# Performance work log

Measured on AMD Instinct MI355X. Metric: run time of the kernel, lower is better.

Reference implementation:

```python
import jax, jax.numpy as jnp
import numpy as np

B, S, DIM = 2, 2048, 1536
H = 12            # n_heads (SIGMA)
HD = DIM // H     # head_dim = 128
SIGMA = 12        # anchors per query: 6 local + 4 strided + 2 global
STRIDE_STEP = 5   # SOPFR


def setup_inputs() -> dict:
    key = jax.random.key(0)
    k0, k1, k2 = jax.random.split(key, 3)
    s = 0.02
    return {
        "x": jax.random.normal(k0, (B, S, DIM), dtype=jnp.float32),
        "Wqkv": jax.random.normal(k1, (DIM, 3 * DIM), dtype=jnp.float32) * s,
        "bqkv": jnp.zeros((3 * DIM,), dtype=jnp.float32),
        "Wout": jax.random.normal(k2, (DIM, DIM), dtype=jnp.float32) * s,
        "bout": jnp.zeros((DIM,), dtype=jnp.float32),
        # Egyptian-fraction init: [W_LOCAL, W_STRIDE, W_GLOBAL] = [1/2, 1/3, 1/6]
        "group_scale": jnp.array([0.5, 1.0 / 3.0, 1.0 / 6.0], dtype=jnp.float32),
    }


def _anchor_indices(seq_len):
    # (S, 12) int32: 6 local offsets, 4 strided offsets, then global {0, S-1}
    pos = jnp.arange(seq_len, dtype=jnp.int32)
    offs = jnp.array([-3, -2, -1, 1, 2, 3,
                      -2 * STRIDE_STEP, -STRIDE_STEP, STRIDE_STEP, 2 * STRIDE_STEP],
                     dtype=jnp.int32)
    a = jnp.clip(pos[:, None] + offs[None, :], 0, seq_len - 1)
    glob = jnp.stack([jnp.zeros_like(pos), jnp.full_like(pos, seq_len - 1)], axis=1)
    return jnp.concatenate([a, glob], axis=1)


def reference(x, Wqkv, bqkv, Wout, bout, group_scale):
    b, s, d_model = x.shape
    # QKV projection -> (3, B, H, S, HD)
    qkv = (x @ Wqkv + bqkv).reshape(b, s, 3, H, HD).transpose(2, 0, 3, 1, 4)
    q, k, v = qkv[0], qkv[1], qkv[2]
    scale = HD ** -0.5

    anchor = _anchor_indices(s)                 # (S, SIGMA)
    k_anchors = jnp.take(k, anchor, axis=2)     # (B, H, S, SIGMA, HD)
    v_anchors = jnp.take(v, anchor, axis=2)     # (B, H, S, SIGMA, HD)

    attn = jnp.einsum('bhsd,bhsad->bhsa', q, k_anchors) * scale

    gw = jax.nn.softmax(group_scale)            # (3,)
    weight_per_anchor = jnp.concatenate([
        jnp.broadcast_to(gw[0], (6,)),   # local
        jnp.broadcast_to(gw[1], (4,)),   # strided
        jnp.broadcast_to(gw[2], (2,)),   # global
    ])                                          # (SIGMA,)
    attn = attn + jnp.log(weight_per_anchor)    # broadcast over (B,H,S,·)

    attn = jax.nn.softmax(attn, axis=-1)
    attn = jnp.nan_to_num(attn, nan=0.0)

    out = jnp.einsum('bhsa,bhsad->bhsd', attn, v_anchors)
    out = out.transpose(0, 2, 1, 3).reshape(b, s, d_model)
    return out @ Wout + bout
```

## Files before the change

### kernel.cpp

```cpp
#include <hip/hip_runtime.h>
#include <hip/hip_bf16.h>
#include <cstdint>
#include <math.h>

#define B_    2
#define S_    2048
#define DIM_  1536
#define H_    12
#define HD_   128
#define TRI_  4608
#define M_    4096

typedef __attribute__((ext_vector_type(8)))  __bf16 bf16x8;
typedef __attribute__((ext_vector_type(4)))  __bf16 bf16x4;
typedef __attribute__((ext_vector_type(4)))  float  floatx4;
typedef __attribute__((ext_vector_type(16))) float  floatx16;

typedef __attribute__((address_space(3))) uint8_t       lds_u8;
typedef const __attribute__((address_space(1))) uint8_t glob_u8;

__global__ __launch_bounds__(256) void prep(const float* __restrict__ W1,
                                            __bf16* __restrict__ O1,
                                            const float* __restrict__ W2,
                                            __bf16* __restrict__ O2,
                                            const float* __restrict__ x,
                                            __bf16* __restrict__ x_bf) {
    const int T1 = (TRI_ / 64) * (DIM_ / 64);
    const int T2 = (DIM_ / 64) * (DIM_ / 64);
    int blk = blockIdx.x;
    const int t = threadIdx.x;

    if (blk >= T1 + T2) {
        blk -= T1 + T2;
        int i = blk * 256 + t;
        float4 v = ((const float4*)x)[i];
        bf16x4 o;
        o.x = (__bf16)v.x; o.y = (__bf16)v.y; o.z = (__bf16)v.z; o.w = (__bf16)v.w;
        *(bf16x4*)(x_bf + (size_t)i * 4) = o;
        return;
    }

    const float* in; __bf16* out; int R, C, c0, r0;
    if (blk < T1) {
        in = W1; out = O1; R = DIM_; C = TRI_;
        c0 = (blk % (TRI_ / 64)) * 64; r0 = (blk / (TRI_ / 64)) * 64;
    } else {
        blk -= T1;
        in = W2; out = O2; R = DIM_; C = DIM_;
        c0 = (blk % (DIM_ / 64)) * 64; r0 = (blk / (DIM_ / 64)) * 64;
    }
    __shared__ float tile[64][65];
    const int c4 = t & 15, r = t >> 4;
    #pragma unroll
    for (int i = 0; i < 64; i += 16) {
        float4 v = *(const float4*)&in[(size_t)(r0 + r + i) * C + c0 + c4 * 4];
        tile[r + i][c4 * 4 + 0] = v.x;
        tile[r + i][c4 * 4 + 1] = v.y;
        tile[r + i][c4 * 4 + 2] = v.z;
        tile[r + i][c4 * 4 + 3] = v.w;
    }
    __syncthreads();
    const int cc = t >> 2, ch = t & 3;
    #pragma unroll
    for (int cho = 0; cho < 8; cho += 4) {
        int chh = ch + cho;
        bf16x8 o;
        #pragma unroll
        for (int k = 0; k < 8; ++k) o[k] = (__bf16)tile[chh * 8 + k][cc];
        *(bf16x8*)&out[(size_t)(c0 + cc) * R + r0 + chh * 8] = o;
    }
}

__global__ __launch_bounds__(256, 3) void gemm_qkv(const __bf16* __restrict__ A,
                                                   const __bf16* __restrict__ Bt,
                                                   const float*  __restrict__ bias,
                                                   __bf16* __restrict__ Cout,
                                                   int Mdim, int Ndim, int Kdim) {
    __shared__ __align__(16) __bf16 sA[128 * 64];
    __shared__ __align__(16) __bf16 sB[192 * 64];

    const int ntiles = Ndim / 192;
    const int tile_n = blockIdx.x % ntiles;
    const int tile_m = blockIdx.x / ntiles;
    const int m0 = tile_m << 7, n0 = tile_n * 192;

    const int tid  = threadIdx.x;
    const int lane = tid & 63;
    const int wave = tid >> 6;
    const int wm = (wave >> 1) * 64;
    const int wn = (wave & 1) * 96;

    floatx16 acc[2][3] = {};

    const int lr8 = lane >> 3;
    const int swz = (((lane & 7) ^ lr8) * 8);

    const int m32  = lane & 31;
    const int half = lane >> 5;
    const int lx7  = lane & 7;

    for (int k0 = 0; k0 < Kdim; k0 += 64) {
        #pragma unroll
        for (int c = 0; c < 4; ++c) {
            int r0 = wave * 32 + c * 8;
            const __bf16* ga = A + (size_t)(m0 + r0 + lr8) * Kdim + k0 + swz;
            __builtin_amdgcn_global_load_lds((glob_u8*)ga, (lds_u8*)&sA[r0 * 64], 16, 0, 0);
        }
        #pragma unroll
        for (int c = 0; c < 6; ++c) {
            int r0 = wave * 48 + c * 8;
            const __bf16* gb = Bt + (size_t)(n0 + r0 + lr8) * Kdim + k0 + swz;
            __builtin_amdgcn_global_load_lds((glob_u8*)gb, (lds_u8*)&sB[r0 * 64], 16, 0, 0);
        }
        __syncthreads();

        #pragma unroll
        for (int ks = 0; ks < 4; ++ks) {
            const int ko = (((ks * 2 + half) ^ lx7) * 8);
            bf16x8 af[2], bfr[3];
            #pragma unroll
            for (int i = 0; i < 2; ++i)
                af[i] = *(const bf16x8*)&sA[(wm + i * 32 + m32) * 64 + ko];
            #pragma unroll
            for (int j = 0; j < 3; ++j)
                bfr[j] = *(const bf16x8*)&sB[(wn + j * 32 + m32) * 64 + ko];
            #pragma unroll
            for (int i = 0; i < 2; ++i)
                #pragma unroll
                for (int j = 0; j < 3; ++j)
                    acc[i][j] = __builtin_amdgcn_mfma_f32_32x32x16_bf16(af[i], bfr[j], acc[i][j], 0, 0, 0);
        }
        __syncthreads();
    }

    #pragma unroll
    for (int j = 0; j < 3; ++j) {
        int gc = n0 + wn + j * 32 + m32;
        float bv = bias[gc];
        #pragma unroll
        for (int i = 0; i < 2; ++i) {
            #pragma unroll
            for (int r = 0; r < 16; ++r) {
                int gr = m0 + wm + i * 32 + (r & 3) + 8 * (r >> 2) + 4 * half;
                Cout[(size_t)gr * Ndim + gc] = (__bf16)(acc[i][j][r] + bv);
            }
        }
    }
}

__global__ __launch_bounds__(256, 3) void gemm_out(const __bf16* __restrict__ A,
                                                   const __bf16* __restrict__ Bt,
                                                   const float*  __restrict__ bias,
                                                   float* __restrict__ Cout,
                                                   int Mdim, int Ndim, int Kdim) {
    __shared__ __align__(16) __bf16 sA[64 * 128];
    __shared__ __align__(16) __bf16 sB[128 * 128];

    const int ntiles = Ndim >> 7;
    const int tile_n = blockIdx.x % ntiles;
    const int tile_m = blockIdx.x / ntiles;
    const int m0 = tile_m << 6, n0 = tile_n << 7;

    const int tid  = threadIdx.x;
    const int lane = tid & 63;
    const int wave = tid >> 6;
    const int wm = (wave >> 1) * 32;
    const int wn = (wave & 1) * 64;

    floatx4 acc[2][4] = {};

    const int lr4 = lane >> 4;
    const int lc  = lane & 15;
    int swz[4];
    #pragma unroll
    for (int v = 0; v < 4; ++v) swz[v] = (lc ^ (v * 4 + lr4)) * 8;

    const int row  = lane & 15;
    const int quad = lane >> 4;

    for (int k0 = 0; k0 < Kdim; k0 += 128) {
        #pragma unroll
        for (int c = 0; c < 4; ++c) {
            int r0 = wave * 16 + c * 4;
            const __bf16* ga = A + (size_t)(m0 + r0 + lr4) * Kdim + k0 + swz[c & 3];
            __builtin_amdgcn_global_load_lds((glob_u8*)ga, (lds_u8*)&sA[r0 * 128], 16, 0, 0);
        }
        #pragma unroll
        for (int c = 0; c < 8; ++c) {
            int r0 = wave * 32 + c * 4;
            const __bf16* gb = Bt + (size_t)(n0 + r0 + lr4) * Kdim + k0 + swz[c & 3];
            __builtin_amdgcn_global_load_lds((glob_u8*)gb, (lds_u8*)&sB[r0 * 128], 16, 0, 0);
        }
        __syncthreads();

        #pragma unroll
        for (int ks = 0; ks < 4; ++ks) {
            const int ck = ((ks * 4 + quad) ^ row) * 8;
            bf16x8 af[2], bfr[4];
            #pragma unroll
            for (int i = 0; i < 2; ++i)
                af[i]  = *(const bf16x8*)&sA[(wm + i * 16 + row) * 128 + ck];
            #pragma unroll
            for (int j = 0; j < 4; ++j)
                bfr[j] = *(const bf16x8*)&sB[(wn + j * 16 + row) * 128 + ck];
            #pragma unroll
            for (int i = 0; i < 2; ++i)
                #pragma unroll
                for (int j = 0; j < 4; ++j)
                    acc[i][j] = __builtin_amdgcn_mfma_f32_16x16x32_bf16(af[i], bfr[j], acc[i][j], 0, 0, 0);
        }
        __syncthreads();
    }

    #pragma unroll
    for (int j = 0; j < 4; ++j) {
        int gc = n0 + wn + j * 16 + row;
        float bv = bias[gc];
        #pragma unroll
        for (int i = 0; i < 2; ++i) {
            #pragma unroll
            for (int r = 0; r < 4; ++r) {
                int gr = m0 + wm + i * 16 + quad * 4 + r;
                Cout[(size_t)gr * Ndim + gc] = acc[i][j][r] + bv;
            }
        }
    }
}

__global__ __launch_bounds__(192) void anchor_attn(const __bf16* __restrict__ qkv,
                                                   const float* __restrict__ group_scale,
                                                   __bf16* __restrict__ attn_out) {
    const int bs = blockIdx.x;
    const int b  = bs >> 11;
    const int s  = bs & 2047;
    const int t  = threadIdx.x;
    const int h  = t >> 4;
    const int tt = t & 15;
    const int d0 = tt * 8;

    float g0 = group_scale[0], g1 = group_scale[1], g2 = group_scale[2];
    float gm = fmaxf(g0, fmaxf(g1, g2));
    float e0 = __expf(g0 - gm), e1 = __expf(g1 - gm), e2 = __expf(g2 - gm);
    float ls = __logf(e0 + e1 + e2);
    float lw0 = g0 - gm - ls, lw1 = g1 - gm - ls, lw2 = g2 - gm - ls;

    const size_t rowbase = (size_t)(b * S_ + s) * TRI_ + h * HD_ + d0;
    bf16x8 qv = *(const bf16x8*)(qkv + rowbase);
    float q[8];
    #pragma unroll
    for (int k = 0; k < 8; ++k) q[k] = (float)qv[k];

    int idxs[12];
    const int offs[10] = {-3, -2, -1, 1, 2, 3, -10, -5, 5, 10};
    #pragma unroll
    for (int a = 0; a < 10; ++a) {
        int tgt = s + offs[a];
        idxs[a] = min(max(tgt, 0), S_ - 1);
    }
    idxs[10] = 0; idxs[11] = S_ - 1;

    const float scale = 0.08838834764831845f;
    float p[12];
    float mx = -1e30f;
    #pragma unroll
    for (int a = 0; a < 12; ++a) {
        const __bf16* kp = qkv + (size_t)(b * S_ + idxs[a]) * TRI_ + DIM_ + h * HD_ + d0;
        bf16x8 kv = *(const bf16x8*)kp;
        float d = 0.f;
        #pragma unroll
        for (int k = 0; k < 8; ++k) d += q[k] * (float)kv[k];
        d += __shfl_xor(d, 1); d += __shfl_xor(d, 2);
        d += __shfl_xor(d, 4); d += __shfl_xor(d, 8);
        float sc = d * scale + (a < 6 ? lw0 : (a < 10 ? lw1 : lw2));
        p[a] = sc;
        mx = fmaxf(mx, sc);
    }
    float l = 0.f;
    #pragma unroll
    for (int a = 0; a < 12; ++a) { p[a] = __expf(p[a] - mx); l += p[a]; }
    float inv = 1.0f / l;

    float o[8] = {};
    #pragma unroll
    for (int a = 0; a < 12; ++a) {
        const __bf16* vp = qkv + (size_t)(b * S_ + idxs[a]) * TRI_ + 2 * DIM_ + h * HD_ + d0;
        bf16x8 vv = *(const bf16x8*)vp;
        #pragma unroll
        for (int k = 0; k < 8; ++k) o[k] += p[a] * (float)vv[k];
    }
    bf16x8 ov;
    #pragma unroll
    for (int k = 0; k < 8; ++k) ov[k] = (__bf16)(o[k] * inv);
    *(bf16x8*)(attn_out + (size_t)(b * S_ + s) * DIM_ + h * HD_ + d0) = ov;
}

extern "C" void kernel_launch(void* const* d_in, const int* in_sizes, int n_in,
                              void* d_out, int out_size, void* d_ws, size_t ws_size,
                              hipStream_t stream) {
    const float* x    = (const float*)d_in[0];
    const float* Wqkv = (const float*)d_in[1];
    const float* bqkv = (const float*)d_in[2];
    const float* Wout = (const float*)d_in[3];
    const float* bout = (const float*)d_in[4];
    const float* gsc  = (const float*)d_in[5];
    float* out = (float*)d_out;

    char* ws = (char*)d_ws;
    __bf16* x_bf   = (__bf16*)(ws);
    __bf16* WqkvT  = (__bf16*)(ws + 12582912);
    __bf16* WoutT  = (__bf16*)(ws + 12582912 + 14155776);
    __bf16* qkv    = (__bf16*)(ws + 12582912 + 14155776 + 4718592);
    __bf16* attn   = (__bf16*)(ws + 12582912 + 14155776 + 4718592 + 37748736);

    {
        int nblk = (TRI_ / 64) * (DIM_ / 64) + (DIM_ / 64) * (DIM_ / 64)
                 + (M_ * DIM_) / 1024;
        prep<<<nblk, 256, 0, stream>>>(Wqkv, WqkvT, Wout, WoutT, x, x_bf);
    }

    gemm_qkv<<<(M_ / 128) * (TRI_ / 192), 256, 0, stream>>>(
        x_bf, WqkvT, bqkv, qkv, M_, TRI_, DIM_);

    anchor_attn<<<B_ * S_, 192, 0, stream>>>(qkv, gsc, attn);

    gemm_out<<<(M_ / 64) * (DIM_ / 128), 256, 0, stream>>>(
        attn, WoutT, bout, out, M_, DIM_, DIM_);
}
```

Measured before the change: 231.2 us.

## Tile anchor attention over 64-query chunks with shared K/V staged in LDS

The attention kernel now processes 64 consecutive queries per (chunk, head, batch) block. It stages the 84-row local window plus the two global rows of K and V into swizzled LDS using global_load_lds, so each anchor row is loaded once per tile instead of being refetched from global memory by every query. Each thread handles 32 dims of one query and reduces across 4 lanes. This trades fewer redundant global reads for LDS traffic and higher register use.

```diff
diff --git a/kernel.cpp b/kernel.cpp
--- a/kernel.cpp
+++ b/kernel.cpp
@@ -227,16 +227,39 @@
     }
 }
 
-__global__ __launch_bounds__(192) void anchor_attn(const __bf16* __restrict__ qkv,
+#define AROWS 86
+#define ATOT  2752
+
+__global__ __launch_bounds__(256) void anchor_attn(const __bf16* __restrict__ qkv,
                                                    const float* __restrict__ group_scale,
                                                    __bf16* __restrict__ attn_out) {
-    const int bs = blockIdx.x;
-    const int b  = bs >> 11;
-    const int s  = bs & 2047;
-    const int t  = threadIdx.x;
-    const int h  = t >> 4;
-    const int tt = t & 15;
-    const int d0 = tt * 8;
+    const int sc = blockIdx.x;
+    const int h  = blockIdx.y;
+    const int b  = blockIdx.z;
+    const int s0 = sc * 64;
+
+    __shared__ __align__(16) __bf16 sKV[2 * AROWS * 128];
+
+    const int tid  = threadIdx.x;
+    const int wave = tid >> 6;
+
+    #pragma unroll
+    for (int base = 0; base < ATOT; base += 256) {
+        int i = base + tid;
+        if (i < ATOT) {
+            int r  = i >> 4;
+            int c  = i & 15;
+            int kv = (r >= AROWS) ? 1 : 0;
+            int rr = r - AROWS * kv;
+            int s_row = (rr < 84) ? min(max(s0 - 10 + rr, 0), S_ - 1)
+                                  : (rr == 84 ? 0 : S_ - 1);
+            int cs = c ^ (rr & 7);
+            const __bf16* src = qkv + (size_t)(b * S_ + s_row) * TRI_
+                              + DIM_ * (1 + kv) + h * HD_ + cs * 8;
+            __builtin_amdgcn_global_load_lds((glob_u8*)src,
+                (lds_u8*)sKV + (size_t)(base + wave * 64) * 16, 16, 0, 0);
+        }
+    }
 
     float g0 = group_scale[0], g1 = group_scale[1], g2 = group_scale[2];
     float gm = fmaxf(g0, fmaxf(g1, g2));
@@ -244,54 +267,75 @@
     float ls = __logf(e0 + e1 + e2);
     float lw0 = g0 - gm - ls, lw1 = g1 - gm - ls, lw2 = g2 - gm - ls;
 
-    const size_t rowbase = (size_t)(b * S_ + s) * TRI_ + h * HD_ + d0;
-    bf16x8 qv = *(const bf16x8*)(qkv + rowbase);
-    float q[8];
-    #pragma unroll
-    for (int k = 0; k < 8; ++k) q[k] = (float)qv[k];
-
-    int idxs[12];
+    const int s_local = tid >> 2;
+    const int ds      = tid & 3;
+    const int s       = s0 + s_local;
+
+    float q[32];
+    {
+        const __bf16* qp = qkv + (size_t)(b * S_ + s) * TRI_ + h * HD_ + ds * 32;
+        #pragma unroll
+        for (int j = 0; j < 4; ++j) {
+            bf16x8 qv = *(const bf16x8*)(qp + j * 8);
+            #pragma unroll
+            for (int k = 0; k < 8; ++k) q[j * 8 + k] = (float)qv[k];
+        }
+    }
+
+    int slot[12];
     const int offs[10] = {-3, -2, -1, 1, 2, 3, -10, -5, 5, 10};
     #pragma unroll
-    for (int a = 0; a < 10; ++a) {
-        int tgt = s + offs[a];
-        idxs[a] = min(max(tgt, 0), S_ - 1);
-    }
-    idxs[10] = 0; idxs[11] = S_ - 1;
+    for (int a = 0; a < 10; ++a) slot[a] = s_local + 10 + offs[a];
+    slot[10] = 84; slot[11] = 85;
+
+    __syncthreads();
 
     const float scale = 0.08838834764831845f;
     float p[12];
     float mx = -1e30f;
     #pragma unroll
     for (int a = 0; a < 12; ++a) {
-        const __bf16* kp = qkv + (size_t)(b * S_ + idxs[a]) * TRI_ + DIM_ + h * HD_ + d0;
-        bf16x8 kv = *(const bf16x8*)kp;
+        const int ro = slot[a] * 128;
+        const int sw = slot[a] & 7;
         float d = 0.f;
         #pragma unroll
-        for (int k = 0; k < 8; ++k) d += q[k] * (float)kv[k];
+        for (int j = 0; j < 4; ++j) {
+            bf16x8 kv = *(const bf16x8*)&sKV[ro + ((ds * 4 + j) ^ sw) * 8];
+            #pragma unroll
+            for (int k = 0; k < 8; ++k) d += q[j * 8 + k] * (float)kv[k];
+        }
         d += __shfl_xor(d, 1); d += __shfl_xor(d, 2);
-        d += __shfl_xor(d, 4); d += __shfl_xor(d, 8);
-        float sc = d * scale + (a < 6 ? lw0 : (a < 10 ? lw1 : lw2));
-        p[a] = sc;
-        mx = fmaxf(mx, sc);
+        float v = d * scale + (a < 6 ? lw0 : (a < 10 ? lw1 : lw2));
+        p[a] = v;
+        mx = fmaxf(mx, v);
     }
     float l = 0.f;
     #pragma unroll
     for (int a = 0; a < 12; ++a) { p[a] = __expf(p[a] - mx); l += p[a]; }
     float inv = 1.0f / l;
 
-    float o[8] = {};
+    float o[32] = {};
     #pragma unroll
     for (int a = 0; a < 12; ++a) {
-        const __bf16* vp = qkv + (size_t)(b * S_ + idxs[a]) * TRI_ + 2 * DIM_ + h * HD_ + d0;
-        bf16x8 vv = *(const bf16x8*)vp;
-        #pragma unroll
-        for (int k = 0; k < 8; ++k) o[k] += p[a] * (float)vv[k];
-    }
-    bf16x8 ov;
-    #pragma unroll
-    for (int k = 0; k < 8; ++k) ov[k] = (__bf16)(o[k] * inv);
-    *(bf16x8*)(attn_out + (size_t)(b * S_ + s) * DIM_ + h * HD_ + d0) = ov;
+        const int ro = AROWS * 128 + slot[a] * 128;
+        const int sw = slot[a] & 7;
+        float pa = p[a];
+        #pragma unroll
+        for (int j = 0; j < 4; ++j) {
+            bf16x8 vv = *(const bf16x8*)&sKV[ro + ((ds * 4 + j) ^ sw) * 8];
+            #pragma unroll
+            for (int k = 0; k < 8; ++k) o[j * 8 + k] += pa * (float)vv[k];
+        }
+    }
+
+    __bf16* op = attn_out + (size_t)(b * S_ + s) * DIM_ + h * HD_ + ds * 32;
+    #pragma unroll
+    for (int j = 0; j < 4; ++j) {
+        bf16x8 ov;
+        #pragma unroll
+        for (int k = 0; k < 8; ++k) ov[k] = (__bf16)(o[j * 8 + k] * inv);
+        *(bf16x8*)(op + j * 8) = ov;
+    }
 }
 
 extern "C" void kernel_launch(void* const* d_in, const int* in_sizes, int n_in,
@@ -321,7 +365,7 @@
     gemm_qkv<<<(M_ / 128) * (TRI_ / 192), 256, 0, stream>>>(
         x_bf, WqkvT, bqkv, qkv, M_, TRI_, DIM_);
 
-    anchor_attn<<<B_ * S_, 192, 0, stream>>>(qkv, gsc, attn);
+    anchor_attn<<<dim3(32, H_, B_), 256, 0, stream>>>(qkv, gsc, attn);
 
     gemm_out<<<(M_ / 64) * (DIM_ / 128), 256, 0, stream>>>(
         attn, WoutT, bout, out, M_, DIM_, DIM_);
```

Result: faster. 210.1 us (-9.1%).
